# Kernel tuning notes

Measured on AMD Instinct MI355X. Metric: run time of the kernel, lower is better.

## Reference

```python
import jax, jax.numpy as jnp
import numpy as np

B_, T_, D_MODEL = 2, 1024, 1024
D_STATE, D_CONV, EXPAND = 16, 4, 2
D_INNER = D_MODEL * EXPAND


def setup_inputs() -> dict:
    key = jax.random.key(0)
    ks = jax.random.split(key, 12)
    def s(k, shape, sc=0.02):
        return jax.random.normal(k, shape, jnp.float32) * sc
    return {
        "x": jax.random.normal(ks[0], (B_, T_, D_MODEL), jnp.float32),
        "ln_g": jnp.ones((D_MODEL,), jnp.float32),
        "ln_b": jnp.zeros((D_MODEL,), jnp.float32),
        "W_in": s(ks[1], (D_MODEL, 2 * D_INNER)),
        "b_in": s(ks[2], (2 * D_INNER,)),
        "conv_w": s(ks[3], (D_INNER, 1, D_CONV)),  # depthwise kernel, torch OIH layout
        "conv_b": s(ks[4], (D_INNER,)),
        "A": s(ks[5], (D_INNER, D_STATE), 0.1),
        "W_B": s(ks[6], (D_INNER, D_STATE)),
        "b_B": s(ks[7], (D_STATE,)),
        "W_C": s(ks[8], (D_INNER, D_STATE)),
        "b_C": s(ks[9], (D_STATE,)),
        "D": jnp.ones((D_INNER,), jnp.float32),
        "W_out": s(ks[10], (D_INNER, D_MODEL)),
        "b_out": s(ks[11], (D_MODEL,)),
    }


def _ssm_forward(x, ln_g, ln_b, W_in, b_in, conv_w, conv_b, A, W_B, b_B, W_C, b_C, D, W_out, b_out):
    eps = 1e-5
    # LayerNorm (biased variance, as in torch)
    mu = jnp.mean(x, axis=-1, keepdims=True)
    var = jnp.var(x, axis=-1, keepdims=True)
    xn = (x - mu) / jnp.sqrt(var + eps) * ln_g + ln_b
    # in_proj -> split into x path and gate
    proj = xn @ W_in + b_in                      # (b, t, 2*d_inner)
    xp, gate = jnp.split(proj, 2, axis=-1)
    # depthwise causal conv1d (padding=d_conv-1 on the left == torch pad + truncate)
    xc = jax.lax.conv_general_dilated(
        xp.transpose(0, 2, 1), conv_w,
        window_strides=(1,), padding=[(D_CONV - 1, 0)],
        dimension_numbers=("NCH", "OIH", "NCH"),
        feature_group_count=D_INNER,
    ).transpose(0, 2, 1) + conv_b                # (b, t, d_inner)
    xc = jax.nn.silu(xc)
    Bt = xc @ W_B + b_B                          # (b, t, d_state)
    Ct = xc @ W_C + b_C                          # (b, t, d_state)
    a = jax.nn.sigmoid(A)                        # (d_inner, d_state), per-channel decay
    u = Bt[:, :, None, :] * xc[:, :, :, None]    # (b, t, d_inner, d_state)
    a_full = jnp.broadcast_to(a, u.shape)
    # h_t = a * h_{t-1} + u_t  via first-order-recurrence associative scan
    def combine(c1, c2):
        a1, u1 = c1
        a2, u2 = c2
        return a2 * a1, a2 * u1 + u2
    _, h = jax.lax.associative_scan(combine, (a_full, u), axis=1)
    y = jnp.einsum("btns,bts->btn", h, Ct) + D * xc
    y = y * jax.nn.silu(gate)
    return y @ W_out + b_out + x                 # residual (dropout is identity in eval)


def reference(x, ln_g, ln_b, W_in, b_in, conv_w, conv_b, A, W_B, b_B, W_C, b_C, D, W_out, b_out):
    return _ssm_forward(x, ln_g, ln_b, W_in, b_in, conv_w, conv_b, A, W_B, b_B, W_C, b_C, D, W_out, b_out)
```

## Files before the change

kernel.cpp:

```cpp
#include <hip/hip_runtime.h>
#include <hip/hip_bf16.h>
#include <stdint.h>

using u16 = unsigned short;
typedef short bf16x8 __attribute__((ext_vector_type(8)));
typedef float f32x4 __attribute__((ext_vector_type(4)));

__device__ __forceinline__ float b2f(u16 u) {
  union { unsigned int i; float f; } v; v.i = ((unsigned int)u) << 16; return v.f;
}
__device__ __forceinline__ u16 f2b(float f) {
  __hip_bfloat16 h = __float2bfloat16(f);
  u16 r; __builtin_memcpy(&r, &h, 2); return r;
}
__device__ __forceinline__ bool probe_bf16(const void* p) {
  return *(const unsigned int*)p == 0x3F803F80u;
}
__device__ __forceinline__ float loadf(const void* p, size_t i, bool bf) {
  return bf ? b2f(((const u16*)p)[i]) : ((const float*)p)[i];
}
__device__ __forceinline__ void gload_lds16(const u16* g, u16* l) {
  __builtin_amdgcn_global_load_lds(
      (const __attribute__((address_space(1))) unsigned int*)(g),
      (__attribute__((address_space(3))) unsigned int*)(l),
      16, 0, 0);
}
template <int BK>
__device__ __forceinline__ int swkey(int row) {
  if constexpr (BK == 32) return (row >> 1) & 3;
  else return row & (BK / 8 - 1);
}

__device__ __forceinline__ void do_transpose(const void* __restrict__ in, u16* __restrict__ out,
                                             int R, int C, int bx, int by, int tid, bool bf) {
  __shared__ u16 tile[32][33];
  int c0 = bx * 32, r0 = by * 32;
  int tx = tid & 31, ty = tid >> 5;
#pragma unroll
  for (int i = 0; i < 4; i++) {
    size_t idx = (size_t)(r0 + ty + i * 8) * C + c0 + tx;
    tile[ty + i * 8][tx] = bf ? ((const u16*)in)[idx] : f2b(((const float*)in)[idx]);
  }
  __syncthreads();
#pragma unroll
  for (int i = 0; i < 4; i++)
    out[(size_t)(c0 + ty + i * 8) * R + r0 + tx] = tile[tx][ty + i * 8];
}

__launch_bounds__(256)
__global__ void prep_kernel(const void* __restrict__ W_in, u16* __restrict__ WinT,
                            const void* __restrict__ W_out, u16* __restrict__ WoutT,
                            const void* __restrict__ WB, const void* __restrict__ WC,
                            u16* __restrict__ WT2, const void* __restrict__ probe) {
  const bool bf = probe_bf16(probe);
  const int bid = blockIdx.x, tid = threadIdx.x;
  if (bid < 4096) {
    do_transpose(W_in, WinT, 1024, 4096, bid & 127, bid >> 7, tid, bf);
  } else if (bid < 6144) {
    int b2 = bid - 4096;
    do_transpose(W_out, WoutT, 2048, 1024, b2 & 31, b2 >> 5, tid, bf);
  } else {
    int g = (bid - 6144) * 256 + tid;
    int c = g & 31, kb = g >> 5;
    const void* W = (c < 16) ? WB : WC;
    int cc = c & 15;
    u16 pk[8];
#pragma unroll
    for (int e = 0; e < 8; e++)
      pk[e] = bf ? ((const u16*)W)[(kb * 8 + e) * 16 + cc]
                 : f2b(((const float*)W)[(kb * 8 + e) * 16 + cc]);
    *(int4*)(WT2 + (size_t)g * 8) = *(int4*)pk;
  }
}

__launch_bounds__(256)
__global__ void ln_kernel(const void* __restrict__ x, const void* __restrict__ g,
                          const void* __restrict__ b, u16* __restrict__ xn) {
  const bool bf = probe_bf16(g);
  const int row = blockIdx.x, tid = threadIdx.x;
  const size_t base = (size_t)row * 1024;
  float v[4]; float s = 0.f, s2 = 0.f;
#pragma unroll
  for (int i = 0; i < 4; i++) {
    v[i] = loadf(x, base + tid + i * 256, bf);
    s += v[i]; s2 += v[i] * v[i];
  }
#pragma unroll
  for (int m = 32; m >= 1; m >>= 1) { s += __shfl_xor(s, m); s2 += __shfl_xor(s2, m); }
  __shared__ float rs[4], rs2[4];
  if ((tid & 63) == 0) { rs[tid >> 6] = s; rs2[tid >> 6] = s2; }
  __syncthreads();
  s = rs[0] + rs[1] + rs[2] + rs[3];
  s2 = rs2[0] + rs2[1] + rs2[2] + rs2[3];
  float mu = s * (1.f / 1024.f);
  float var = s2 * (1.f / 1024.f) - mu * mu;
  float rstd = rsqrtf(var + 1e-5f);
#pragma unroll
  for (int i = 0; i < 4; i++) {
    int c = tid + i * 256;
    float o = (v[i] - mu) * rstd * loadf(g, c, bf) + loadf(b, c, bf);
    xn[base + c] = f2b(o);
  }
}

template <int ROWS, int BK>
__device__ __forceinline__ void stage_tile(const u16* __restrict__ g, u16* lbuf,
                                           int K, int wave, int lane) {
  constexpr int LPR = BK / 8;
  constexpr int RPI = 512 / BK;
  constexpr int NI = ROWS / RPI;
  const int lr = lane / LPR, lc = lane % LPR;
#pragma unroll
  for (int j = wave; j < NI; j += 4) {
    int row = j * RPI + lr;
    int col = (lc ^ swkey<BK>(row)) * 8;
    gload_lds16(g + (size_t)row * K + col, lbuf + (size_t)j * RPI * BK);
  }
}

template <int BM, int BN, int BK, bool RESID, bool DUALOUT, bool PARTIAL>
__launch_bounds__(256)
__global__ void gemm_async(const u16* __restrict__ A, const u16* __restrict__ BT,
                           const void* __restrict__ bias, const void* __restrict__ resid,
                           void* __restrict__ Cout, float* __restrict__ Cpart,
                           int M, int N, int K, int k_len,
                           const void* __restrict__ probe) {
  constexpr int WM = BM / 2, WN = BN / 2;
  constexpr int TM = WM / 16, TN = WN / 16;
  constexpr int KF = BK / 32;
  __shared__ __align__(16) u16 lds[2][(BM + BN) * BK];
  const int tid = threadIdx.x;
  const int bm = blockIdx.x, bn = blockIdx.y, bz = blockIdx.z;
  const int lane = tid & 63, wave = tid >> 6;
  const int wm = wave >> 1, wn = wave & 1;
  const int lrow = lane & 15, quad = lane >> 4;
  f32x4 acc[TM][TN] = {};
  const u16* Ag = A + (size_t)bm * BM * K + (size_t)bz * k_len;
  const u16* Bg = BT + (size_t)bn * BN * K + (size_t)bz * k_len;

  stage_tile<BM, BK>(Ag, &lds[0][0], K, wave, lane);
  stage_tile<BN, BK>(Bg, &lds[0][BM * BK], K, wave, lane);
  __syncthreads();

  int cur = 0;
  for (int k0 = 0; k0 < k_len; k0 += BK, cur ^= 1) {
    if (k0 + BK < k_len) {
      stage_tile<BM, BK>(Ag + k0 + BK, &lds[cur ^ 1][0], K, wave, lane);
      stage_tile<BN, BK>(Bg + k0 + BK, &lds[cur ^ 1][BM * BK], K, wave, lane);
    }
    const u16* bufA = &lds[cur][0];
    const u16* bufB = &lds[cur][BM * BK];
#pragma unroll
    for (int f = 0; f < KF; f++) {
      bf16x8 af[TM], bv[TN];
#pragma unroll
      for (int i = 0; i < TM; i++) {
        int row = wm * WM + i * 16 + lrow;
        af[i] = *(const bf16x8*)&bufA[(size_t)row * BK + (((f * 4 + quad) ^ swkey<BK>(row)) * 8)];
      }
#pragma unroll
      for (int j = 0; j < TN; j++) {
        int row = wn * WN + j * 16 + lrow;
        bv[j] = *(const bf16x8*)&bufB[(size_t)row * BK + (((f * 4 + quad) ^ swkey<BK>(row)) * 8)];
      }
#pragma unroll
      for (int i = 0; i < TM; i++)
#pragma unroll
        for (int j = 0; j < TN; j++)
          acc[i][j] = __builtin_amdgcn_mfma_f32_16x16x32_bf16(af[i], bv[j], acc[i][j], 0, 0, 0);
    }
    __syncthreads();
  }

  if constexpr (PARTIAL) {
    float* P = Cpart + (size_t)bz * M * N;
#pragma unroll
    for (int i = 0; i < TM; i++)
#pragma unroll
      for (int j = 0; j < TN; j++) {
        int col = bn * BN + wn * WN + j * 16 + lrow;
#pragma unroll
        for (int r = 0; r < 4; r++) {
          int row = bm * BM + wm * WM + i * 16 + quad * 4 + r;
          P[(size_t)row * N + col] = acc[i][j][r];
        }
      }
    return;
  }

  const bool bf = probe_bf16(probe);
#pragma unroll
  for (int i = 0; i < TM; i++) {
#pragma unroll
    for (int j = 0; j < TN; j++) {
      int col = bn * BN + wn * WN + j * 16 + lrow;
      float bvv = loadf(bias, col, bf);
#pragma unroll
      for (int r = 0; r < 4; r++) {
        int row = bm * BM + wm * WM + i * 16 + quad * 4 + r;
        float v = acc[i][j][r] + bvv;
        if constexpr (RESID) v += loadf(resid, (size_t)row * N + col, bf);
        if constexpr (DUALOUT) {
          if (bf) ((u16*)Cout)[(size_t)row * N + col] = f2b(v);
          else    ((float*)Cout)[(size_t)row * N + col] = v;
        } else {
          ((u16*)Cout)[(size_t)row * N + col] = f2b(v);
        }
      }
    }
  }
}

__launch_bounds__(256)
__global__ void reduce_out(const float* __restrict__ p, const void* __restrict__ bias,
                           const void* __restrict__ resid, void* __restrict__ out,
                           const void* __restrict__ probe) {
  const bool bf = probe_bf16(probe);
  const int row = blockIdx.x, c0 = threadIdx.x * 4;
  const size_t i = (size_t)row * 1024 + c0;
  f32x4 a = *(const f32x4*)(p + i);
  f32x4 b = *(const f32x4*)(p + (size_t)2048 * 1024 + i);
  float o[4];
#pragma unroll
  for (int e = 0; e < 4; e++)
    o[e] = a[e] + b[e] + loadf(bias, c0 + e, bf) + loadf(resid, i + e, bf);
  if (bf) {
    u16 pk[4];
#pragma unroll
    for (int e = 0; e < 4; e++) pk[e] = f2b(o[e]);
    *(uint2*)((u16*)out + i) = *(uint2*)pk;
  } else {
    f32x4 v; v[0] = o[0]; v[1] = o[1]; v[2] = o[2]; v[3] = o[3];
    *(f32x4*)((float*)out + i) = v;
  }
}

__launch_bounds__(256)
__global__ void conv_bc2(const u16* __restrict__ proj, const void* __restrict__ cw,
                         const void* __restrict__ cb, const u16* __restrict__ WT2,
                         const void* __restrict__ bB, const void* __restrict__ bC,
                         u16* __restrict__ xcb, float* __restrict__ BC,
                         const void* __restrict__ probe) {
  const bool bf = probe_bf16(probe);
  __shared__ __align__(16) float xr[2048];
  __shared__ float red[8][33];
  const int row = blockIdx.x, tid = threadIdx.x;
  const int t = row & 1023;
  const int n0 = tid * 8;
  float acc[8], w[8][4];
#pragma unroll
  for (int e = 0; e < 8; e++) {
    acc[e] = loadf(cb, n0 + e, bf);
#pragma unroll
    for (int k = 0; k < 4; k++) w[e][k] = loadf(cw, (size_t)(n0 + e) * 4 + k, bf);
  }
#pragma unroll
  for (int k = 0; k < 4; k++) {
    if (t - 3 + k >= 0) {
      union { int4 v; u16 u[8]; } uu;
      uu.v = *(const int4*)(proj + (size_t)(row - 3 + k) * 4096 + n0);
#pragma unroll
      for (int e = 0; e < 8; e++)
        acc[e] = __builtin_fmaf(b2f(uu.u[e]), w[e][k], acc[e]);
    }
  }
  {
    union { int4 v; u16 u[8]; } pk;
    f32x4 lo, hi;
#pragma unroll
    for (int e = 0; e < 8; e++) {
      float s = acc[e];
      float xv = s / (1.f + __expf(-s));
      if (e < 4) lo[e] = xv; else hi[e - 4] = xv;
      pk.u[e] = f2b(xv);
    }
    *(f32x4*)&xr[n0] = lo;
    *(f32x4*)&xr[n0 + 4] = hi;
    *(int4*)(xcb + (size_t)row * 2048 + n0) = pk.v;
  }
  __syncthreads();
  const int c = tid & 31, sl = tid >> 5;
  const float* xk = &xr[sl * 256];
  float p = 0.f;
#pragma unroll 4
  for (int j = 0; j < 32; j++) {
    int kb = sl * 32 + j;
    union { int4 v; u16 u[8]; } w8;
    w8.v = *(const int4*)(WT2 + ((size_t)kb * 32 + c) * 8);
    f32x4 x0 = *(const f32x4*)(xk + j * 8);
    f32x4 x1 = *(const f32x4*)(xk + j * 8 + 4);
#pragma unroll
    for (int e = 0; e < 4; e++) {
      p = __builtin_fmaf(x0[e], b2f(w8.u[e]), p);
      p = __builtin_fmaf(x1[e], b2f(w8.u[4 + e]), p);
    }
  }
  red[sl][c] = p;
  __syncthreads();
  if (tid < 32) {
    float s = 0.f;
#pragma unroll
    for (int i = 0; i < 8; i++) s += red[i][tid];
    s += (tid < 16) ? loadf(bB, tid, bf) : loadf(bC, tid - 16, bf);
    BC[(size_t)row * 32 + tid] = s;
  }
}


__launch_bounds__(256)
__global__ void scan_pass1(const u16* __restrict__ xc, const float* __restrict__ BC,
                           const void* __restrict__ Abuf, float* __restrict__ carry,
                           const void* __restrict__ probe) {
  const bool bf = probe_bf16(probe);
  const int tid = threadIdx.x;
  const int c = blockIdx.x & 31, ng = (blockIdx.x >> 5) & 7, bi = blockIdx.x >> 8;
  const int n = ng * 256 + tid;
  float a[16], h[16];
#pragma unroll
  for (int s = 0; s < 16; s++) {
    float av = loadf(Abuf, n * 16 + s, bf);
    a[s] = 1.f / (1.f + __expf(-av));
    h[s] = 0.f;
  }
  __shared__ __align__(16) u16 xs[32 * 256];
  __shared__ __align__(16) float bcs[32 * 32];
  const u16* xcp = xc + (size_t)bi * 1024 * 2048 + ng * 256;
  const float* bcp = BC + (size_t)bi * 1024 * 32;
  const int tc = c * 32;
#pragma unroll
  for (int i = 0; i < 4; i++) {
    int ch = tid + i * 256;
    int r = ch >> 5, cv = (ch & 31) * 8;
    *(int4*)&xs[ch * 8] = *(const int4*)(xcp + (size_t)(tc + r) * 2048 + cv);
  }
  {
    int r = tid >> 3, cv = (tid & 7) * 4;
    *(int4*)&bcs[tid * 4] = *(const int4*)(bcp + (size_t)(tc + r) * 32 + cv);
  }
  __syncthreads();
  for (int t = 0; t < 32; t++) {
    float x = b2f(xs[t * 256 + tid]);
#pragma unroll
    for (int s = 0; s < 16; s++)
      h[s] = __builtin_fmaf(a[s], h[s], bcs[t * 32 + s] * x);
  }
  float* cp = carry + ((size_t)(bi * 32 + c) * 2048 + n) * 16;
#pragma unroll
  for (int s = 0; s < 16; s++) cp[s] = h[s];
}

__launch_bounds__(256)
__global__ void scan_prefix(float* __restrict__ carry, const void* __restrict__ Abuf,
                            const void* __restrict__ probe) {
  const bool bf = probe_bf16(probe);
  const int g = blockIdx.x * 256 + threadIdx.x;
  const int s = g & 15, n = (g >> 4) & 2047, bi = g >> 15;
  float a = 1.f / (1.f + __expf(-loadf(Abuf, n * 16 + s, bf)));
  float aL = a;
#pragma unroll
  for (int i = 0; i < 5; i++) aL = aL * aL;
  float running = 0.f;
  for (int c = 0; c < 32; c++) {
    size_t idx = ((size_t)(bi * 32 + c) * 2048 + n) * 16 + s;
    float tmp = carry[idx];
    carry[idx] = running;
    running = __builtin_fmaf(aL, running, tmp);
  }
}

__launch_bounds__(256)
__global__ void scan_pass2(const u16* __restrict__ xc, const u16* __restrict__ proj,
                           const float* __restrict__ BC, const void* __restrict__ Abuf,
                           const void* __restrict__ Dbuf, const float* __restrict__ carry,
                           u16* __restrict__ ybar, const void* __restrict__ probe) {
  const bool bf = probe_bf16(probe);
  const int tid = threadIdx.x;
  const int c = blockIdx.x & 31, ng = (blockIdx.x >> 5) & 7, bi = blockIdx.x >> 8;
  const int n = ng * 256 + tid;
  float a[16], h[16];
  const float* cp = carry + ((size_t)(bi * 32 + c) * 2048 + n) * 16;
#pragma unroll
  for (int s = 0; s < 16; s++) {
    float av = loadf(Abuf, n * 16 + s, bf);
    a[s] = 1.f / (1.f + __expf(-av));
    h[s] = cp[s];
  }
  const float Dn = loadf(Dbuf, n, bf);
  __shared__ __align__(16) u16 xs[32 * 256];
  __shared__ __align__(16) u16 gs[32 * 256];
  __shared__ __align__(16) float bcs[32 * 32];
  const u16* xcp = xc + (size_t)bi * 1024 * 2048 + ng * 256;
  const u16* gp = proj + (size_t)bi * 1024 * 4096 + 2048 + ng * 256;
  const float* bcp = BC + (size_t)bi * 1024 * 32;
  u16* yp = ybar + (size_t)bi * 1024 * 2048 + ng * 256;
  const int tc = c * 32;
#pragma unroll
  for (int i = 0; i < 4; i++) {
    int ch = tid + i * 256;
    int r = ch >> 5, cv = (ch & 31) * 8;
    *(int4*)&xs[ch * 8] = *(const int4*)(xcp + (size_t)(tc + r) * 2048 + cv);
    *(int4*)&gs[ch * 8] = *(const int4*)(gp + (size_t)(tc + r) * 4096 + cv);
  }
  {
    int r = tid >> 3, cv = (tid & 7) * 4;
    *(int4*)&bcs[tid * 4] = *(const int4*)(bcp + (size_t)(tc + r) * 32 + cv);
  }
  __syncthreads();
  for (int t = 0; t < 32; t++) {
    float x = b2f(xs[t * 256 + tid]);
    float acc = 0.f;
#pragma unroll
    for (int s = 0; s < 16; s++) {
      h[s] = __builtin_fmaf(a[s], h[s], bcs[t * 32 + s] * x);
      acc = __builtin_fmaf(h[s], bcs[t * 32 + 16 + s], acc);
    }
    float y = acc + Dn * x;
    float g = b2f(gs[t * 256 + tid]);
    float yg = y * g / (1.f + __expf(-g));
    yp[(size_t)(tc + t) * 2048 + tid] = f2b(yg);
  }
}

extern "C" void kernel_launch(void* const* d_in, const int* in_sizes, int n_in,
                              void* d_out, int out_size, void* d_ws, size_t ws_size,
                              hipStream_t stream) {
  const void* x = d_in[0];
  const void* ln_g = d_in[1];
  const void* ln_b = d_in[2];
  const void* W_in = d_in[3];
  const void* b_in = d_in[4];
  const void* conv_w = d_in[5];
  const void* conv_b = d_in[6];
  const void* A = d_in[7];
  const void* W_B = d_in[8];
  const void* b_B = d_in[9];
  const void* W_C = d_in[10];
  const void* b_C = d_in[11];
  const void* Dp = d_in[12];
  const void* W_out = d_in[13];
  const void* b_out = d_in[14];
  const void* probe = ln_g;

  char* ws = (char*)d_ws;
  u16* WinT = (u16*)ws;
  u16* ybar = (u16*)ws;
  u16* xn = (u16*)(ws + (size_t)8 * 1024 * 1024);
  u16* proj = (u16*)(ws + (size_t)12 * 1024 * 1024);
  u16* xcb = (u16*)(ws + (size_t)28 * 1024 * 1024);
  float* BC = (float*)(ws + (size_t)36 * 1024 * 1024);
  float* carry = (float*)(ws + (size_t)36 * 1024 * 1024 + 256 * 1024);
  u16* WT2 = (u16*)(ws + (size_t)46 * 1024 * 1024);
  float* part = (float*)(ws + (size_t)48 * 1024 * 1024);
  u16* WoutT = (u16*)(ws + (size_t)64 * 1024 * 1024);

  prep_kernel<<<6176, 256, 0, stream>>>(W_in, WinT, W_out, WoutT, W_B, W_C, WT2, probe);
  ln_kernel<<<2048, 256, 0, stream>>>(x, ln_g, ln_b, xn);
  gemm_async<128, 128, 64, false, false, false><<<dim3(16, 32), 256, 0, stream>>>(
      xn, WinT, b_in, nullptr, proj, nullptr, 2048, 4096, 1024, 1024, probe);
  conv_bc2<<<2048, 256, 0, stream>>>(proj, conv_w, conv_b, WT2, b_B, b_C, xcb, BC, probe);
  scan_pass1<<<512, 256, 0, stream>>>(xcb, BC, A, carry, probe);
  scan_prefix<<<256, 256, 0, stream>>>(carry, A, probe);
  scan_pass2<<<512, 256, 0, stream>>>(xcb, proj, BC, A, Dp, carry, ybar, probe);
  gemm_async<128, 64, 64, false, false, true><<<dim3(16, 16, 2), 256, 0, stream>>>(
      ybar, WoutT, nullptr, nullptr, nullptr, part, 2048, 1024, 2048, 1024, probe);
  reduce_out<<<2048, 256, 0, stream>>>(part, b_out, x, d_out, probe);
}
```

Before: 250.6 us.

## Split conv+BC projection into conv kernel plus split-K MFMA GEMM and reduce

Replaces the fused conv+SiLU+B/C projection kernel with three kernels: an elementwise causal conv+SiLU, a split-K bf16 MFMA GEMM computing the 32 B/C columns into partial buffers, and a reduction that adds biases. The B/C weight is repacked as a transposed [32][2048] bf16 matrix to suit the GEMM tile loader. The aim is to move the scalar FMA dot products onto matrix cores. In exchange it adds two kernel launches, a partial-sum buffer round trip, and makes the conv kernel do scalar 2-byte loads. The B/C inputs now come from bf16-rounded xc rather than fp32.

```diff
diff --git a/kernel.cpp b/kernel.cpp
--- a/kernel.cpp
+++ b/kernel.cpp
@@ -51,7 +51,7 @@
 __global__ void prep_kernel(const void* __restrict__ W_in, u16* __restrict__ WinT,
                             const void* __restrict__ W_out, u16* __restrict__ WoutT,
                             const void* __restrict__ WB, const void* __restrict__ WC,
-                            u16* __restrict__ WT2, const void* __restrict__ probe) {
+                            u16* __restrict__ WTbc, const void* __restrict__ probe) {
   const bool bf = probe_bf16(probe);
   const int bid = blockIdx.x, tid = threadIdx.x;
   if (bid < 4096) {
@@ -61,15 +61,15 @@
     do_transpose(W_out, WoutT, 2048, 1024, b2 & 31, b2 >> 5, tid, bf);
   } else {
     int g = (bid - 6144) * 256 + tid;
-    int c = g & 31, kb = g >> 5;
+    int c = g >> 8, k0 = (g & 255) * 8;
     const void* W = (c < 16) ? WB : WC;
     int cc = c & 15;
     u16 pk[8];
 #pragma unroll
     for (int e = 0; e < 8; e++)
-      pk[e] = bf ? ((const u16*)W)[(kb * 8 + e) * 16 + cc]
-                 : f2b(((const float*)W)[(kb * 8 + e) * 16 + cc]);
-    *(int4*)(WT2 + (size_t)g * 8) = *(int4*)pk;
+      pk[e] = bf ? ((const u16*)W)[(size_t)(k0 + e) * 16 + cc]
+                 : f2b(((const float*)W)[(size_t)(k0 + e) * 16 + cc]);
+    *(int4*)(WTbc + (size_t)c * 2048 + k0) = *(int4*)pk;
   }
 }
 
@@ -235,77 +235,96 @@
   }
 }
 
-__launch_bounds__(256)
-__global__ void conv_bc2(const u16* __restrict__ proj, const void* __restrict__ cw,
-                         const void* __restrict__ cb, const u16* __restrict__ WT2,
-                         const void* __restrict__ bB, const void* __restrict__ bC,
-                         u16* __restrict__ xcb, float* __restrict__ BC,
-                         const void* __restrict__ probe) {
-  const bool bf = probe_bf16(probe);
-  __shared__ __align__(16) float xr[2048];
-  __shared__ float red[8][33];
-  const int row = blockIdx.x, tid = threadIdx.x;
+__global__ void conv_silu_kernel(const u16* __restrict__ proj, const void* __restrict__ cw,
+                                 const void* __restrict__ cb, u16* __restrict__ xc,
+                                 const void* __restrict__ probe) {
+  const bool bf = probe_bf16(probe);
+  const int n = blockIdx.x * 256 + threadIdx.x;
+  const int row = blockIdx.y;
   const int t = row & 1023;
-  const int n0 = tid * 8;
-  float acc[8], w[8][4];
-#pragma unroll
-  for (int e = 0; e < 8; e++) {
-    acc[e] = loadf(cb, n0 + e, bf);
-#pragma unroll
-    for (int k = 0; k < 4; k++) w[e][k] = loadf(cw, (size_t)(n0 + e) * 4 + k, bf);
-  }
+  float w[4];
+#pragma unroll
+  for (int k = 0; k < 4; k++) w[k] = loadf(cw, n * 4 + k, bf);
+  float s = loadf(cb, n, bf);
 #pragma unroll
   for (int k = 0; k < 4; k++) {
-    if (t - 3 + k >= 0) {
-      union { int4 v; u16 u[8]; } uu;
-      uu.v = *(const int4*)(proj + (size_t)(row - 3 + k) * 4096 + n0);
-#pragma unroll
-      for (int e = 0; e < 8; e++)
-        acc[e] = __builtin_fmaf(b2f(uu.u[e]), w[e][k], acc[e]);
-    }
-  }
-  {
-    union { int4 v; u16 u[8]; } pk;
-    f32x4 lo, hi;
-#pragma unroll
-    for (int e = 0; e < 8; e++) {
-      float s = acc[e];
-      float xv = s / (1.f + __expf(-s));
-      if (e < 4) lo[e] = xv; else hi[e - 4] = xv;
-      pk.u[e] = f2b(xv);
-    }
-    *(f32x4*)&xr[n0] = lo;
-    *(f32x4*)&xr[n0 + 4] = hi;
-    *(int4*)(xcb + (size_t)row * 2048 + n0) = pk.v;
-  }
-  __syncthreads();
-  const int c = tid & 31, sl = tid >> 5;
-  const float* xk = &xr[sl * 256];
-  float p = 0.f;
-#pragma unroll 4
-  for (int j = 0; j < 32; j++) {
-    int kb = sl * 32 + j;
-    union { int4 v; u16 u[8]; } w8;
-    w8.v = *(const int4*)(WT2 + ((size_t)kb * 32 + c) * 8);
-    f32x4 x0 = *(const f32x4*)(xk + j * 8);
-    f32x4 x1 = *(const f32x4*)(xk + j * 8 + 4);
-#pragma unroll
-    for (int e = 0; e < 4; e++) {
-      p = __builtin_fmaf(x0[e], b2f(w8.u[e]), p);
-      p = __builtin_fmaf(x1[e], b2f(w8.u[4 + e]), p);
-    }
-  }
-  red[sl][c] = p;
-  __syncthreads();
-  if (tid < 32) {
-    float s = 0.f;
-#pragma unroll
-    for (int i = 0; i < 8; i++) s += red[i][tid];
-    s += (tid < 16) ? loadf(bB, tid, bf) : loadf(bC, tid - 16, bf);
-    BC[(size_t)row * 32 + tid] = s;
-  }
-}
-
+    int tt = t - 3 + k;
+    if (tt >= 0) s += b2f(proj[(size_t)(row - 3 + k) * 4096 + n]) * w[k];
+  }
+  float sg = 1.f / (1.f + __expf(-s));
+  xc[(size_t)row * 2048 + n] = f2b(s * sg);
+}
+
+__launch_bounds__(256)
+__global__ void gemm_bc(const u16* __restrict__ A, const u16* __restrict__ WT,
+                        float* __restrict__ part) {
+  constexpr int BK = 64, KLEN = 128;
+  __shared__ __align__(16) u16 lds[2][(128 + 32) * BK];
+  const int tid = threadIdx.x;
+  const int bm = blockIdx.x, bz = blockIdx.y;
+  const int lane = tid & 63, wave = tid >> 6;
+  const int lrow = lane & 15, quad = lane >> 4;
+  f32x4 acc[2][2] = {};
+  const u16* Ag = A + (size_t)bm * 128 * 2048 + bz * KLEN;
+  const u16* Bg = WT + bz * KLEN;
+
+  stage_tile<128, BK>(Ag, &lds[0][0], 2048, wave, lane);
+  stage_tile<32, BK>(Bg, &lds[0][128 * BK], 2048, wave, lane);
+  __syncthreads();
+  int cur = 0;
+  for (int k0 = 0; k0 < KLEN; k0 += BK, cur ^= 1) {
+    if (k0 + BK < KLEN) {
+      stage_tile<128, BK>(Ag + k0 + BK, &lds[cur ^ 1][0], 2048, wave, lane);
+      stage_tile<32, BK>(Bg + k0 + BK, &lds[cur ^ 1][128 * BK], 2048, wave, lane);
+    }
+    const u16* bufA = &lds[cur][0];
+    const u16* bufB = &lds[cur][128 * BK];
+#pragma unroll
+    for (int f = 0; f < 2; f++) {
+      bf16x8 af[2], bv[2];
+#pragma unroll
+      for (int i = 0; i < 2; i++) {
+        int row = wave * 32 + i * 16 + lrow;
+        af[i] = *(const bf16x8*)&bufA[(size_t)row * BK + (((f * 4 + quad) ^ (row & 7)) * 8)];
+      }
+#pragma unroll
+      for (int j = 0; j < 2; j++) {
+        int row = j * 16 + lrow;
+        bv[j] = *(const bf16x8*)&bufB[(size_t)row * BK + (((f * 4 + quad) ^ (row & 7)) * 8)];
+      }
+#pragma unroll
+      for (int i = 0; i < 2; i++)
+#pragma unroll
+        for (int j = 0; j < 2; j++)
+          acc[i][j] = __builtin_amdgcn_mfma_f32_16x16x32_bf16(af[i], bv[j], acc[i][j], 0, 0, 0);
+    }
+    __syncthreads();
+  }
+#pragma unroll
+  for (int i = 0; i < 2; i++)
+#pragma unroll
+    for (int j = 0; j < 2; j++) {
+      int col = j * 16 + lrow;
+#pragma unroll
+      for (int r = 0; r < 4; r++) {
+        int row = bm * 128 + wave * 32 + i * 16 + quad * 4 + r;
+        part[((size_t)bz * 2048 + row) * 32 + col] = acc[i][j][r];
+      }
+    }
+}
+
+__launch_bounds__(256)
+__global__ void reduce_bc(const float* __restrict__ part, const void* __restrict__ bB,
+                          const void* __restrict__ bC, float* __restrict__ BC,
+                          const void* __restrict__ probe) {
+  const bool bf = probe_bf16(probe);
+  const int g = blockIdx.x * 256 + threadIdx.x;
+  const int c = g & 31;
+  float s = (c < 16) ? loadf(bB, c, bf) : loadf(bC, c - 16, bf);
+#pragma unroll
+  for (int z = 0; z < 16; z++) s += part[(size_t)z * 65536 + g];
+  BC[g] = s;
+}
 
 __launch_bounds__(256)
 __global__ void scan_pass1(const u16* __restrict__ xc, const float* __restrict__ BC,
@@ -449,15 +468,18 @@
   u16* xcb = (u16*)(ws + (size_t)28 * 1024 * 1024);
   float* BC = (float*)(ws + (size_t)36 * 1024 * 1024);
   float* carry = (float*)(ws + (size_t)36 * 1024 * 1024 + 256 * 1024);
-  u16* WT2 = (u16*)(ws + (size_t)46 * 1024 * 1024);
+  u16* WTbc = (u16*)(ws + (size_t)46 * 1024 * 1024);
   float* part = (float*)(ws + (size_t)48 * 1024 * 1024);
   u16* WoutT = (u16*)(ws + (size_t)64 * 1024 * 1024);
-
-  prep_kernel<<<6176, 256, 0, stream>>>(W_in, WinT, W_out, WoutT, W_B, W_C, WT2, probe);
+  float* part_bc = (float*)(ws + (size_t)68 * 1024 * 1024);
+
+  prep_kernel<<<6176, 256, 0, stream>>>(W_in, WinT, W_out, WoutT, W_B, W_C, WTbc, probe);
   ln_kernel<<<2048, 256, 0, stream>>>(x, ln_g, ln_b, xn);
   gemm_async<128, 128, 64, false, false, false><<<dim3(16, 32), 256, 0, stream>>>(
       xn, WinT, b_in, nullptr, proj, nullptr, 2048, 4096, 1024, 1024, probe);
-  conv_bc2<<<2048, 256, 0, stream>>>(proj, conv_w, conv_b, WT2, b_B, b_C, xcb, BC, probe);
+  conv_silu_kernel<<<dim3(8, 2048), 256, 0, stream>>>(proj, conv_w, conv_b, xcb, probe);
+  gemm_bc<<<dim3(16, 16), 256, 0, stream>>>(xcb, WTbc, part_bc);
+  reduce_bc<<<256, 256, 0, stream>>>(part_bc, b_B, b_C, BC, probe);
   scan_pass1<<<512, 256, 0, stream>>>(xcb, BC, A, carry, probe);
   scan_prefix<<<256, 256, 0, stream>>>(carry, A, probe);
   scan_pass2<<<512, 256, 0, stream>>>(xcb, proj, BC, A, Dp, carry, ybar, probe);
```

Measured after the change: 219.3 us. 12.5% less time.
